# Performance work log

Hardware: AMD Instinct MI355X
Metric: run time of the kernel (lower is better)

## Reference

```python
import jax, jax.numpy as jnp
from jax import lax
import numpy as np

V, H, D, B, W = 256, 512, 2, 256, 256  # vector_size, hidden_size, depth, batch, window_size


def setup_inputs() -> dict:
    key = jax.random.key(0)
    ks = jax.random.split(key, 13)
    scale = 0.04  # ~ 1/sqrt(hidden)
    names = ["w_ih_ltr", "w_hh_ltr", "b_ih_ltr", "b_hh_ltr", "w_fc_ltr", "b_fc_ltr",
             "w_ih_rtl", "w_hh_rtl", "b_ih_rtl", "b_hh_rtl", "w_fc_rtl", "b_fc_rtl"]
    shapes = [(D, 4 * H, V), (D, 4 * H, H), (D, 4 * H), (D, 4 * H), (D, V, H), (D, V)] * 2
    inp = {"x": jax.random.normal(ks[0], (B, W, V), dtype=jnp.float32)}
    for i, (n, s) in enumerate(zip(names, shapes)):
        inp[n] = jax.random.normal(ks[i + 1], s, dtype=jnp.float32) * scale
    return inp


def _lstm_cell(x, h, c, wih, whh, bih, bhh):
    # PyTorch gate order: i, f, g, o
    g = x @ wih.T + bih + h @ whh.T + bhh
    i, f, gg, o = jnp.split(g, 4, axis=-1)
    c = jax.nn.sigmoid(f) * c + jax.nn.sigmoid(i) * jnp.tanh(gg)
    h = jax.nn.sigmoid(o) * jnp.tanh(c)
    return h, c


def _run_dir(xs, wih, whh, bih, bhh, wfc, bfc):
    # xs: (T, B, V); depth LSTM(1-step)+FC blocks with persistent (h,c) per depth
    depth = wih.shape[0]
    h0 = jnp.zeros((depth, xs.shape[1], whh.shape[-1]), xs.dtype)

    def step(carry, x):
        h, c = carry
        v = x
        hs, cs = [], []
        for j in range(depth):  # small fixed depth loop
            hj, cj = _lstm_cell(v, h[j], c[j], wih[j], whh[j], bih[j], bhh[j])
            v = hj @ wfc[j].T + bfc[j]
            hs.append(hj)
            cs.append(cj)
        return (jnp.stack(hs), jnp.stack(cs)), v

    _, ys = lax.scan(step, (h0, h0), xs)
    return ys  # (T, B, V)


def reference(x, w_ih_ltr, w_hh_ltr, b_ih_ltr, b_hh_ltr, w_fc_ltr, b_fc_ltr,
              w_ih_rtl, w_hh_rtl, b_ih_rtl, b_hh_rtl, w_fc_rtl, b_fc_rtl):
    Wlen = x.shape[1]
    xs_f = jnp.swapaxes(x[:, :Wlen - 1, :], 0, 1)        # steps i = 0 .. W-2
    xs_b = jnp.swapaxes(x[:, Wlen - 1:0:-1, :], 0, 1)    # steps -(i+1) = W-1 .. 1
    ys_f = _run_dir(xs_f, w_ih_ltr, w_hh_ltr, b_ih_ltr, b_hh_ltr, w_fc_ltr, b_fc_ltr)
    ys_b = _run_dir(xs_b, w_ih_rtl, w_hh_rtl, b_ih_rtl, b_hh_rtl, w_fc_rtl, b_fc_rtl)
    # torch.stack(output, dim=1): forward outputs then backward outputs -> (B, 2*(W-1), V)
    return jnp.swapaxes(jnp.concatenate([ys_f, ys_b], axis=0), 0, 1)
```

## Files before the change

### kernel.cpp

```cpp
#include <hip/hip_runtime.h>
#include <hip/hip_bf16.h>

using bf16   = __bf16;
using bf16x8 = __attribute__((ext_vector_type(8))) __bf16;
using f32x4  = __attribute__((ext_vector_type(4))) float;
using u32x4  = __attribute__((ext_vector_type(4))) unsigned int;

#define TSTEPS 255
#define UNITE  512
#define HPAR   (16*16*512)
#define WA_UNITS_DIR (128*24)
#define WB_UNITS_DIR (128*32)
#define WC_UNITS_DIR (16*16)

#define MFMA(acc, a, b) acc = __builtin_amdgcn_mfma_f32_16x16x32_bf16((a), (b), (acc), 0, 0, 0)

__device__ __forceinline__ float sigmoidf_(float x) { return 1.f / (1.f + __expf(-x)); }
__device__ __forceinline__ float tanhf_(float x) {
    float e = __expf(-2.f * fabsf(x));
    float t = (1.f - e) / (1.f + e);
    return copysignf(t, x);
}

__device__ __forceinline__ void load8_coh(const bf16* ph, const bf16* pl,
                                          u32x4* h, u32x4* l) {
    asm volatile(
        "global_load_dwordx4 %0, %8, off sc0 sc1\n\t"
        "global_load_dwordx4 %1, %8, off offset:1024 sc0 sc1\n\t"
        "global_load_dwordx4 %2, %8, off offset:2048 sc0 sc1\n\t"
        "global_load_dwordx4 %3, %8, off offset:3072 sc0 sc1\n\t"
        "global_load_dwordx4 %4, %9, off sc0 sc1\n\t"
        "global_load_dwordx4 %5, %9, off offset:1024 sc0 sc1\n\t"
        "global_load_dwordx4 %6, %9, off offset:2048 sc0 sc1\n\t"
        "global_load_dwordx4 %7, %9, off offset:3072 sc0 sc1\n\t"
        "s_waitcnt vmcnt(0)"
        : "=&v"(h[0]), "=&v"(h[1]), "=&v"(h[2]), "=&v"(h[3]),
          "=&v"(l[0]), "=&v"(l[1]), "=&v"(l[2]), "=&v"(l[3])
        : "v"(ph), "v"(pl)
        : "memory");
}

__device__ __forceinline__ void storeh_coh(bf16* ph, bf16* pl,
                                           unsigned short vh, unsigned short vl) {
    asm volatile(
        "global_store_short %0, %2, off sc0 sc1\n\t"
        "global_store_short %1, %3, off sc0 sc1"
        :: "v"(ph), "v"(pl), "v"(vh), "v"(vl)
        : "memory");
}

__device__ __forceinline__ void split_store8(const float* __restrict__ src,
                                             bf16* __restrict__ dh, bf16* __restrict__ dl) {
    float f[8];
    *(float4*)f       = *(const float4*)src;
    *(float4*)(f + 4) = *(const float4*)(src + 4);
    bf16x8 oh, ol;
    #pragma unroll
    for (int j = 0; j < 8; ++j) { bf16 h = (bf16)f[j]; oh[j] = h; ol[j] = (bf16)(f[j] - (float)h); }
    *(bf16x8*)dh = oh; *(bf16x8*)dl = ol;
}

__device__ __forceinline__ void gbarrier(unsigned* __restrict__ flags, int bid, unsigned epoch) {
    asm volatile("s_waitcnt vmcnt(0)" ::: "memory");
    __syncthreads();
    if (threadIdx.x == 0)
        asm volatile("global_store_dword %0, %1, off sc0 sc1"
                     :: "v"(&flags[bid]), "v"(epoch) : "memory");
    if (threadIdx.x < 64) {
        const int l = threadIdx.x;
        for (;;) {
            unsigned f0 = __hip_atomic_load(&flags[l],       __ATOMIC_RELAXED, __HIP_MEMORY_SCOPE_AGENT);
            unsigned f1 = __hip_atomic_load(&flags[l + 64],  __ATOMIC_RELAXED, __HIP_MEMORY_SCOPE_AGENT);
            unsigned f2 = __hip_atomic_load(&flags[l + 128], __ATOMIC_RELAXED, __HIP_MEMORY_SCOPE_AGENT);
            unsigned f3 = __hip_atomic_load(&flags[l + 192], __ATOMIC_RELAXED, __HIP_MEMORY_SCOPE_AGENT);
            if (__all(f0 >= epoch && f1 >= epoch && f2 >= epoch && f3 >= epoch)) break;
            __builtin_amdgcn_s_sleep(1);
        }
    }
    __syncthreads();
}


__global__ void k_pack_wa(const float* __restrict__ wihL, const float* __restrict__ whhL,
                          const float* __restrict__ wihR, const float* __restrict__ whhR,
                          bf16* __restrict__ wah, bf16* __restrict__ wal) {
    int gid = blockIdx.x * 256 + threadIdx.x;
    int lane = gid & 63, u = gid >> 6;
    int kb = u % 24; int tn = (u / 24) & 127; int dir = u / 3072;
    int r = lane & 15, q = lane >> 4;
    int n = tn * 16 + r, k = kb * 32 + q * 8;
    const float* wih = dir ? wihR : wihL;
    const float* whh = dir ? whhR : whhL;
    const float* src = (k < 256) ? (wih + (size_t)n * 256 + k)
                                 : (whh + (size_t)n * 512 + (k - 256));
    split_store8(src, wah + (size_t)u * UNITE + lane * 8, wal + (size_t)u * UNITE + lane * 8);
}

__global__ void k_wcomb(const float* __restrict__ wihL, const float* __restrict__ wfcL,
                        const float* __restrict__ wihR, const float* __restrict__ wfcR,
                        float* __restrict__ wcf) {
    size_t gid = (size_t)blockIdx.x * 256 + threadIdx.x;
    int k = gid & 511; int n = (gid >> 9) & 2047; int dir = (int)(gid >> 20);
    const float* wih1 = (dir ? wihR : wihL) + (size_t)2048 * 256;
    const float* wfc0 = (dir ? wfcR : wfcL);
    float s = 0.f;
    #pragma unroll 8
    for (int v = 0; v < 256; ++v)
        s = fmaf(wih1[(size_t)n * 256 + v], wfc0[(size_t)v * 512 + k], s);
    wcf[gid] = s;
}

__global__ void k_pack_wb(const float* __restrict__ whhL, const float* __restrict__ whhR,
                          const float* __restrict__ wcf,
                          bf16* __restrict__ wbh, bf16* __restrict__ wbl) {
    int gid = blockIdx.x * 256 + threadIdx.x;
    int lane = gid & 63, u = gid >> 6;
    int kb = u & 31, tn = (u >> 5) & 127, dir = u >> 12;
    int r = lane & 15, q = lane >> 4;
    int n = tn * 16 + r, k = kb * 32 + q * 8;
    const float* src;
    if (k < 512) {
        src = wcf + ((size_t)dir * 2048 + n) * 512 + k;
    } else {
        const float* whh1 = (dir ? whhR : whhL) + (size_t)2048 * 512;
        src = whh1 + (size_t)n * 512 + (k - 512);
    }
    split_store8(src, wbh + (size_t)u * UNITE + lane * 8, wbl + (size_t)u * UNITE + lane * 8);
}

__global__ void k_pack_wc(const float* __restrict__ wfcL, const float* __restrict__ wfcR,
                          bf16* __restrict__ wch, bf16* __restrict__ wcl) {
    int gid = blockIdx.x * 256 + threadIdx.x;
    int lane = gid & 63, u = gid >> 6;
    int kb = u & 15, tn = (u >> 4) & 15, dir = u >> 8;
    int r = lane & 15, q = lane >> 4;
    int n = tn * 16 + r, k = kb * 32 + q * 8;
    const float* wfc1 = (dir ? wfcR : wfcL) + (size_t)256 * 512;
    split_store8(wfc1 + (size_t)n * 512 + k,
                 wch + (size_t)u * UNITE + lane * 8, wcl + (size_t)u * UNITE + lane * 8);
}

__global__ void k_bias(const float* __restrict__ bihL, const float* __restrict__ bhhL,
                       const float* __restrict__ bfcL, const float* __restrict__ wihL,
                       const float* __restrict__ bihR, const float* __restrict__ bhhR,
                       const float* __restrict__ bfcR, const float* __restrict__ wihR,
                       float* __restrict__ ba, float* __restrict__ bb, float* __restrict__ bc) {
    int gid = blockIdx.x * 256 + threadIdx.x;
    int n = gid & 2047, dir = gid >> 11;
    const float* bih = dir ? bihR : bihL;
    const float* bhh = dir ? bhhR : bhhL;
    const float* bfc = dir ? bfcR : bfcL;
    const float* wih1 = (dir ? wihR : wihL) + (size_t)2048 * 256;
    ba[dir * 2048 + n] = bih[n] + bhh[n];
    float s = bih[2048 + n] + bhh[2048 + n];
    #pragma unroll 8
    for (int v = 0; v < 256; ++v)
        s = fmaf(bfc[v], wih1[(size_t)n * 256 + v], s);
    bb[dir * 2048 + n] = s;
    if (n < 256) bc[dir * 256 + n] = bfc[256 + n];
}

__global__ __launch_bounds__(256) void bilstm_main(
    const float* __restrict__ x,
    const bf16* __restrict__ wah, const bf16* __restrict__ wal,
    const bf16* __restrict__ wbh, const bf16* __restrict__ wbl,
    const bf16* __restrict__ wch, const bf16* __restrict__ wcl,
    bf16* __restrict__ h0pk, bf16* __restrict__ h1pk,
    const float* __restrict__ ba, const float* __restrict__ bb,
    const float* __restrict__ bc, float* __restrict__ out,
    unsigned* __restrict__ flags)
{
    const int bid  = blockIdx.x;
    const int xcd  = bid & 7;
    const int slot = bid >> 3;
    const int mq   = slot >> 3;
    const int p8   = slot & 7;
    const int pairidx = xcd * 8 + p8;
    const int dir  = pairidx & 1;
    const int nslc = pairidx >> 1;
    const int wv   = threadIdx.x >> 6;
    const int lane = threadIdx.x & 63;
    const int r = lane & 15, q = lane >> 4;
    const int tm = mq * 4 + wv;

    const bf16* WAh = wah + (size_t)dir * WA_UNITS_DIR * UNITE;
    const bf16* WAl = wal + (size_t)dir * WA_UNITS_DIR * UNITE;
    const bf16* WBh = wbh + (size_t)dir * WB_UNITS_DIR * UNITE;
    const bf16* WBl = wbl + (size_t)dir * WB_UNITS_DIR * UNITE;
    const bf16* WCh = wch + (size_t)dir * WC_UNITS_DIR * UNITE;
    const bf16* WCl = wcl + (size_t)dir * WC_UNITS_DIR * UNITE;
    bf16* H0 = h0pk + (size_t)dir * 4 * HPAR;
    bf16* H1 = h1pk + (size_t)dir * 4 * HPAR;
    const float* BA = ba + dir * 2048;
    const float* BB = bb + dir * 2048;
    const float* BC = bc + dir * 256;

    const int col = nslc * 16 + r;
    const int blkK = col >> 5;
    const int kl = col & 31;
    const size_t hw_base = (size_t)(tm * 16 + blkK) * UNITE
                         + (size_t)(kl >> 3) * 128 + (size_t)(4 * q) * 8 + (kl & 7);

    const float bia0 = BA[col], bia1 = BA[512 + col], bia2 = BA[1024 + col], bia3 = BA[1536 + col];
    const float bib0 = BB[col], bib1 = BB[512 + col], bib2 = BB[1024 + col], bib3 = BB[1536 + col];

    const int yid = (nslc * 4 + mq) * 4 + wv;
    const int ytm = yid & 15, ytn = (yid >> 4) & 15, ykh = yid >> 8;
    const float byc = (ykh == 0) ? BC[ytn * 16 + r] : 0.f;

    f32x4 c0 = {0.f, 0.f, 0.f, 0.f}, c1 = {0.f, 0.f, 0.f, 0.f};
    unsigned epoch = 0;

    for (int t = 0; t <= TSTEPS; ++t) {
        const int pw = t & 1, pr = pw ^ 1;
        if (t < TSTEPS) {
            const int pos = dir ? (255 - t) : t;
            f32x4 acc[4] = {{0,0,0,0},{0,0,0,0},{0,0,0,0},{0,0,0,0}};
            const float* xp = x + ((size_t)(tm * 16 + r) * 256 + pos) * 256 + q * 8;
            const bf16* ahh_p = H0 + (size_t)pr * 2 * HPAR + (size_t)(tm * 16) * UNITE + lane * 8;
            const bf16* ahl_p = ahh_p + HPAR;
            #pragma unroll
            for (int kb = 0; kb < 8; ++kb) {
                float xf[8];
                *(float4*)xf       = *(const float4*)(xp + kb * 32);
                *(float4*)(xf + 4) = *(const float4*)(xp + kb * 32 + 4);
                bf16x8 axh, axl;
                #pragma unroll
                for (int j = 0; j < 8; ++j) { bf16 h = (bf16)xf[j]; axh[j] = h; axl[j] = (bf16)(xf[j] - (float)h); }
                #pragma unroll
                for (int g = 0; g < 4; ++g) {
                    const size_t wu = ((size_t)((g * 32 + nslc) * 24) + kb) * UNITE + lane * 8;
                    bf16x8 bh = *(const bf16x8*)(WAh + wu);
                    bf16x8 bl = *(const bf16x8*)(WAl + wu);
                    MFMA(acc[g], axh, bh); MFMA(acc[g], axh, bl); MFMA(acc[g], axl, bh);
                }
            }
            #pragma unroll
            for (int kb0 = 0; kb0 < 16; kb0 += 4) {
                u32x4 th[4], tl[4];
                load8_coh(ahh_p + (size_t)kb0 * UNITE, ahl_p + (size_t)kb0 * UNITE, th, tl);
                #pragma unroll
                for (int j = 0; j < 4; ++j) {
                    bf16x8 hh = __builtin_bit_cast(bf16x8, th[j]);
                    bf16x8 hl = __builtin_bit_cast(bf16x8, tl[j]);
                    const int kb = kb0 + j;
                    #pragma unroll
                    for (int g = 0; g < 4; ++g) {
                        const size_t wu = ((size_t)((g * 32 + nslc) * 24) + 8 + kb) * UNITE + lane * 8;
                        bf16x8 bh = *(const bf16x8*)(WAh + wu);
                        bf16x8 bl = *(const bf16x8*)(WAl + wu);
                        MFMA(acc[g], hh, bh); MFMA(acc[g], hh, bl); MFMA(acc[g], hl, bh);
                    }
                }
            }
            bf16* HwH = H0 + (size_t)pw * 2 * HPAR;
            bf16* HwL = HwH + HPAR;
            #pragma unroll
            for (int i = 0; i < 4; ++i) {
                float gi = sigmoidf_(acc[0][i] + bia0);
                float gf = sigmoidf_(acc[1][i] + bia1);
                float gg = tanhf_   (acc[2][i] + bia2);
                float go = sigmoidf_(acc[3][i] + bia3);
                float cc = gf * c0[i] + gi * gg;
                c0[i] = cc;
                float hv = go * tanhf_(cc);
                bf16 hh = (bf16)hv;
                bf16 hl = (bf16)(hv - (float)hh);
                storeh_coh(HwH + hw_base + (size_t)i * 8, HwL + hw_base + (size_t)i * 8,
                           __builtin_bit_cast(unsigned short, hh),
                           __builtin_bit_cast(unsigned short, hl));
            }
        }
        if (t >= 1) {
            const int py = (t - 1) & 1;
            f32x4 acc = {0, 0, 0, 0};
            const bf16* ayh = H1 + (size_t)py * 2 * HPAR
                            + (size_t)(ytm * 16 + ykh * 8) * UNITE + lane * 8;
            const bf16* ayl = ayh + HPAR;
            #pragma unroll
            for (int kk0 = 0; kk0 < 8; kk0 += 4) {
                u32x4 th[4], tl[4];
                load8_coh(ayh + (size_t)kk0 * UNITE, ayl + (size_t)kk0 * UNITE, th, tl);
                #pragma unroll
                for (int j = 0; j < 4; ++j) {
                    const int kb = ykh * 8 + kk0 + j;
                    const size_t wu = (size_t)(ytn * 16 + kb) * UNITE + lane * 8;
                    bf16x8 bh = *(const bf16x8*)(WCh + wu);
                    bf16x8 bl = *(const bf16x8*)(WCl + wu);
                    bf16x8 ah = __builtin_bit_cast(bf16x8, th[j]);
                    bf16x8 al = __builtin_bit_cast(bf16x8, tl[j]);
                    MFMA(acc, ah, bh); MFMA(acc, ah, bl); MFMA(acc, al, bh);
                }
            }
            const int tout = dir ? (255 + (t - 1)) : (t - 1);
            #pragma unroll
            for (int i = 0; i < 4; ++i) {
                size_t oidx = ((size_t)(ytm * 16 + 4 * q + i) * 510 + tout) * 256 + (ytn * 16 + r);
                atomicAdd(out + oidx, acc[i] + byc);
            }
        }
        ++epoch; gbarrier(flags, bid, epoch);
        if (t < TSTEPS) {
            f32x4 acc[4] = {{0,0,0,0},{0,0,0,0},{0,0,0,0},{0,0,0,0}};
            const bf16* a0h = H0 + (size_t)pw * 2 * HPAR + (size_t)(tm * 16) * UNITE + lane * 8;
            const bf16* a0l = a0h + HPAR;
            const bf16* a1h = H1 + (size_t)pr * 2 * HPAR + (size_t)(tm * 16) * UNITE + lane * 8;
            const bf16* a1l = a1h + HPAR;
            #pragma unroll
            for (int kb0 = 0; kb0 < 16; kb0 += 4) {
                u32x4 th[4], tl[4];
                load8_coh(a0h + (size_t)kb0 * UNITE, a0l + (size_t)kb0 * UNITE, th, tl);
                #pragma unroll
                for (int j = 0; j < 4; ++j) {
                    bf16x8 hh = __builtin_bit_cast(bf16x8, th[j]);
                    bf16x8 hl = __builtin_bit_cast(bf16x8, tl[j]);
                    const int kb = kb0 + j;
                    #pragma unroll
                    for (int g = 0; g < 4; ++g) {
                        const size_t wu = ((size_t)((g * 32 + nslc) * 32) + kb) * UNITE + lane * 8;
                        bf16x8 bh = *(const bf16x8*)(WBh + wu);
                        bf16x8 bl = *(const bf16x8*)(WBl + wu);
                        MFMA(acc[g], hh, bh); MFMA(acc[g], hh, bl); MFMA(acc[g], hl, bh);
                    }
                }
            }
            #pragma unroll
            for (int kb0 = 0; kb0 < 16; kb0 += 4) {
                u32x4 th[4], tl[4];
                load8_coh(a1h + (size_t)kb0 * UNITE, a1l + (size_t)kb0 * UNITE, th, tl);
                #pragma unroll
                for (int j = 0; j < 4; ++j) {
                    bf16x8 hh = __builtin_bit_cast(bf16x8, th[j]);
                    bf16x8 hl = __builtin_bit_cast(bf16x8, tl[j]);
                    const int kb = kb0 + j;
                    #pragma unroll
                    for (int g = 0; g < 4; ++g) {
                        const size_t wu = ((size_t)((g * 32 + nslc) * 32) + 16 + kb) * UNITE + lane * 8;
                        bf16x8 bh = *(const bf16x8*)(WBh + wu);
                        bf16x8 bl = *(const bf16x8*)(WBl + wu);
                        MFMA(acc[g], hh, bh); MFMA(acc[g], hh, bl); MFMA(acc[g], hl, bh);
                    }
                }
            }
            bf16* HwH = H1 + (size_t)pw * 2 * HPAR;
            bf16* HwL = HwH + HPAR;
            #pragma unroll
            for (int i = 0; i < 4; ++i) {
                float gi = sigmoidf_(acc[0][i] + bib0);
                float gf = sigmoidf_(acc[1][i] + bib1);
                float gg = tanhf_   (acc[2][i] + bib2);
                float go = sigmoidf_(acc[3][i] + bib3);
                float cc = gf * c1[i] + gi * gg;
                c1[i] = cc;
                float hv = go * tanhf_(cc);
                bf16 hh = (bf16)hv;
                bf16 hl = (bf16)(hv - (float)hh);
                storeh_coh(HwH + hw_base + (size_t)i * 8, HwL + hw_base + (size_t)i * 8,
                           __builtin_bit_cast(unsigned short, hh),
                           __builtin_bit_cast(unsigned short, hl));
            }
        }
        ++epoch; gbarrier(flags, bid, epoch);
    }
}

extern "C" void kernel_launch(void* const* d_in, const int* in_sizes, int n_in,
                              void* d_out, int out_size, void* d_ws, size_t ws_size,
                              hipStream_t stream) {
    (void)in_sizes; (void)n_in; (void)ws_size;
    const float* x    = (const float*)d_in[0];
    const float* wihL = (const float*)d_in[1];
    const float* whhL = (const float*)d_in[2];
    const float* bihL = (const float*)d_in[3];
    const float* bhhL = (const float*)d_in[4];
    const float* wfcL = (const float*)d_in[5];
    const float* bfcL = (const float*)d_in[6];
    const float* wihR = (const float*)d_in[7];
    const float* whhR = (const float*)d_in[8];
    const float* bihR = (const float*)d_in[9];
    const float* bhhR = (const float*)d_in[10];
    const float* wfcR = (const float*)d_in[11];
    const float* bfcR = (const float*)d_in[12];

    char* ws = (char*)d_ws;
    size_t off = 0;
    auto take = [&](size_t bytes) -> char* {
        off = (off + 255) & ~(size_t)255;
        char* p = ws + off;
        off += bytes;
        return p;
    };
    bf16*     WAH = (bf16*)take((size_t)2 * WA_UNITS_DIR * 1024);
    bf16*     WAL = (bf16*)take((size_t)2 * WA_UNITS_DIR * 1024);
    bf16*     WBH = (bf16*)take((size_t)2 * WB_UNITS_DIR * 1024);
    bf16*     WBL = (bf16*)take((size_t)2 * WB_UNITS_DIR * 1024);
    bf16*     WCH = (bf16*)take((size_t)2 * WC_UNITS_DIR * 1024);
    bf16*     WCL = (bf16*)take((size_t)2 * WC_UNITS_DIR * 1024);
    bf16*     H0  = (bf16*)take((size_t)8 * HPAR * 2);
    bf16*     H1  = (bf16*)take((size_t)8 * HPAR * 2);
    float*    WCF = (float*)take((size_t)2 * 2048 * 512 * 4);
    float*    BA  = (float*)take((size_t)2 * 2048 * 4);
    float*    BB  = (float*)take((size_t)2 * 2048 * 4);
    float*    BC  = (float*)take((size_t)2 * 256 * 4);
    unsigned* FLG = (unsigned*)take((size_t)256 * 4);

    hipMemsetAsync(H0, 0, (size_t)8 * HPAR * 2, stream);
    hipMemsetAsync(H1, 0, (size_t)8 * HPAR * 2, stream);
    hipMemsetAsync(FLG, 0, (size_t)256 * 4, stream);
    hipMemsetAsync(d_out, 0, (size_t)out_size * 4, stream);

    k_pack_wa<<<1536, 256, 0, stream>>>(wihL, whhL, wihR, whhR, WAH, WAL);
    k_wcomb  <<<8192, 256, 0, stream>>>(wihL, wfcL, wihR, wfcR, WCF);
    k_pack_wb<<<2048, 256, 0, stream>>>(whhL, whhR, WCF, WBH, WBL);
    k_pack_wc<<<128,  256, 0, stream>>>(wfcL, wfcR, WCH, WCL);
    k_bias   <<<16,   256, 0, stream>>>(bihL, bhhL, bfcL, wihL, bihR, bhhR, bfcR, wihR, BA, BB, BC);

    bilstm_main<<<256, 256, 0, stream>>>(x, WAH, WAL, WBH, WBL, WCH, WCL,
                                         H0, H1, BA, BB, BC, (float*)d_out, FLG);
}
```

Measured before the change: 32.82 ms.

## Remap blocks to batch-tile ownership and stage hidden states through LDS

```diff
diff --git a/kernel.cpp b/kernel.cpp
--- a/kernel.cpp
+++ b/kernel.cpp
@@ -20,24 +20,6 @@
     float e = __expf(-2.f * fabsf(x));
     float t = (1.f - e) / (1.f + e);
     return copysignf(t, x);
-}
-
-__device__ __forceinline__ void load8_coh(const bf16* ph, const bf16* pl,
-                                          u32x4* h, u32x4* l) {
-    asm volatile(
-        "global_load_dwordx4 %0, %8, off sc0 sc1\n\t"
-        "global_load_dwordx4 %1, %8, off offset:1024 sc0 sc1\n\t"
-        "global_load_dwordx4 %2, %8, off offset:2048 sc0 sc1\n\t"
-        "global_load_dwordx4 %3, %8, off offset:3072 sc0 sc1\n\t"
-        "global_load_dwordx4 %4, %9, off sc0 sc1\n\t"
-        "global_load_dwordx4 %5, %9, off offset:1024 sc0 sc1\n\t"
-        "global_load_dwordx4 %6, %9, off offset:2048 sc0 sc1\n\t"
-        "global_load_dwordx4 %7, %9, off offset:3072 sc0 sc1\n\t"
-        "s_waitcnt vmcnt(0)"
-        : "=&v"(h[0]), "=&v"(h[1]), "=&v"(h[2]), "=&v"(h[3]),
-          "=&v"(l[0]), "=&v"(l[1]), "=&v"(l[2]), "=&v"(l[3])
-        : "v"(ph), "v"(pl)
-        : "memory");
 }
 
 __device__ __forceinline__ void storeh_coh(bf16* ph, bf16* pl,
@@ -47,6 +29,42 @@
         "global_store_short %1, %3, off sc0 sc1"
         :: "v"(ph), "v"(pl), "v"(vh), "v"(vl)
         : "memory");
+}
+
+__device__ __forceinline__ void stage32k(const bf16* gh, const bf16* gl,
+                                         bf16* lds, int tid) {
+    u32x4 a0, a1, a2, a3, b0, b1, b2, b3;
+    const bf16* p0 = gh + tid * 8;
+    const bf16* p1 = p0 + 2048;
+    const bf16* p2 = p0 + 4096;
+    const bf16* p3 = p0 + 6144;
+    const bf16* q0 = gl + tid * 8;
+    const bf16* q1 = q0 + 2048;
+    const bf16* q2 = q0 + 4096;
+    const bf16* q3 = q0 + 6144;
+    asm volatile(
+        "global_load_dwordx4 %0, %8, off sc0 sc1\n\t"
+        "global_load_dwordx4 %1, %9, off sc0 sc1\n\t"
+        "global_load_dwordx4 %2, %10, off sc0 sc1\n\t"
+        "global_load_dwordx4 %3, %11, off sc0 sc1\n\t"
+        "global_load_dwordx4 %4, %12, off sc0 sc1\n\t"
+        "global_load_dwordx4 %5, %13, off sc0 sc1\n\t"
+        "global_load_dwordx4 %6, %14, off sc0 sc1\n\t"
+        "global_load_dwordx4 %7, %15, off sc0 sc1\n\t"
+        "s_waitcnt vmcnt(0)"
+        : "=&v"(a0), "=&v"(a1), "=&v"(a2), "=&v"(a3),
+          "=&v"(b0), "=&v"(b1), "=&v"(b2), "=&v"(b3)
+        : "v"(p0), "v"(p1), "v"(p2), "v"(p3),
+          "v"(q0), "v"(q1), "v"(q2), "v"(q3)
+        : "memory");
+    *(u32x4*)(lds + tid * 8)                 = a0;
+    *(u32x4*)(lds + tid * 8 + 2048)          = a1;
+    *(u32x4*)(lds + tid * 8 + 4096)          = a2;
+    *(u32x4*)(lds + tid * 8 + 6144)          = a3;
+    *(u32x4*)(lds + 8192 + tid * 8)          = b0;
+    *(u32x4*)(lds + 8192 + tid * 8 + 2048)   = b1;
+    *(u32x4*)(lds + 8192 + tid * 8 + 4096)   = b2;
+    *(u32x4*)(lds + 8192 + tid * 8 + 6144)   = b3;
 }
 
 __device__ __forceinline__ void split_store8(const float* __restrict__ src,
@@ -171,17 +189,16 @@
     unsigned* __restrict__ flags)
 {
     const int bid  = blockIdx.x;
-    const int xcd  = bid & 7;
-    const int slot = bid >> 3;
-    const int mq   = slot >> 3;
-    const int p8   = slot & 7;
-    const int pairidx = xcd * 8 + p8;
-    const int dir  = pairidx & 1;
-    const int nslc = pairidx >> 1;
-    const int wv   = threadIdx.x >> 6;
-    const int lane = threadIdx.x & 63;
+    const int nslc = bid & 7;
+    const int bq   = (bid >> 3) & 15;
+    const int dir  = bid >> 7;
+    const int tid  = threadIdx.x;
+    const int wv   = tid >> 6;
+    const int lane = tid & 63;
     const int r = lane & 15, q = lane >> 4;
-    const int tm = mq * 4 + wv;
+
+    __shared__ __align__(16) bf16 h0s[16384];
+    __shared__ __align__(16) bf16 h1s[16384];
 
     const bf16* WAh = wah + (size_t)dir * WA_UNITS_DIR * UNITE;
     const bf16* WAl = wal + (size_t)dir * WA_UNITS_DIR * UNITE;
@@ -195,30 +212,32 @@
     const float* BB = bb + dir * 2048;
     const float* BC = bc + dir * 256;
 
-    const int col = nslc * 16 + r;
-    const int blkK = col >> 5;
-    const int kl = col & 31;
-    const size_t hw_base = (size_t)(tm * 16 + blkK) * UNITE
-                         + (size_t)(kl >> 3) * 128 + (size_t)(4 * q) * 8 + (kl & 7);
-
+    const int nbase = nslc * 4 + wv;
+    const int col   = nslc * 64 + wv * 16 + r;
     const float bia0 = BA[col], bia1 = BA[512 + col], bia2 = BA[1024 + col], bia3 = BA[1536 + col];
     const float bib0 = BB[col], bib1 = BB[512 + col], bib2 = BB[1024 + col], bib3 = BB[1536 + col];
 
-    const int yid = (nslc * 4 + mq) * 4 + wv;
-    const int ytm = yid & 15, ytn = (yid >> 4) & 15, ykh = yid >> 8;
-    const float byc = (ykh == 0) ? BC[ytn * 16 + r] : 0.f;
+    const int hunit  = bq * 16 + nslc * 2 + (wv >> 1);
+    const int hw_off = ((wv & 1) * 2 + (r >> 3)) * 128 + q * 32 + (r & 7);
+
+    const int tn  = nslc * 2 + (wv & 1);
+    const float byc = BC[tn * 16 + r];
 
     f32x4 c0 = {0.f, 0.f, 0.f, 0.f}, c1 = {0.f, 0.f, 0.f, 0.f};
     unsigned epoch = 0;
 
+    #pragma unroll
+    for (int k2 = 0; k2 < 8; ++k2) *(u32x4*)(h0s + tid * 8 + k2 * 2048) = (u32x4){0, 0, 0, 0};
+    __syncthreads();
+
     for (int t = 0; t <= TSTEPS; ++t) {
         const int pw = t & 1, pr = pw ^ 1;
+        stage32k(H1 + (size_t)pr * 2 * HPAR + (size_t)bq * 8192,
+                 H1 + (size_t)pr * 2 * HPAR + HPAR + (size_t)bq * 8192, h1s, tid);
         if (t < TSTEPS) {
             const int pos = dir ? (255 - t) : t;
             f32x4 acc[4] = {{0,0,0,0},{0,0,0,0},{0,0,0,0},{0,0,0,0}};
-            const float* xp = x + ((size_t)(tm * 16 + r) * 256 + pos) * 256 + q * 8;
-            const bf16* ahh_p = H0 + (size_t)pr * 2 * HPAR + (size_t)(tm * 16) * UNITE + lane * 8;
-            const bf16* ahl_p = ahh_p + HPAR;
+            const float* xp = x + ((size_t)(bq * 16 + r) * 256 + pos) * 256 + q * 8;
             #pragma unroll
             for (int kb = 0; kb < 8; ++kb) {
                 float xf[8];
@@ -229,32 +248,26 @@
                 for (int j = 0; j < 8; ++j) { bf16 h = (bf16)xf[j]; axh[j] = h; axl[j] = (bf16)(xf[j] - (float)h); }
                 #pragma unroll
                 for (int g = 0; g < 4; ++g) {
-                    const size_t wu = ((size_t)((g * 32 + nslc) * 24) + kb) * UNITE + lane * 8;
+                    const size_t wu = ((size_t)((g * 32 + nbase) * 24 + kb)) * UNITE + lane * 8;
                     bf16x8 bh = *(const bf16x8*)(WAh + wu);
                     bf16x8 bl = *(const bf16x8*)(WAl + wu);
                     MFMA(acc[g], axh, bh); MFMA(acc[g], axh, bl); MFMA(acc[g], axl, bh);
                 }
             }
             #pragma unroll
-            for (int kb0 = 0; kb0 < 16; kb0 += 4) {
-                u32x4 th[4], tl[4];
-                load8_coh(ahh_p + (size_t)kb0 * UNITE, ahl_p + (size_t)kb0 * UNITE, th, tl);
+            for (int hk = 0; hk < 16; ++hk) {
+                bf16x8 ah = *(const bf16x8*)(h0s + hk * 512 + lane * 8);
+                bf16x8 al = *(const bf16x8*)(h0s + 8192 + hk * 512 + lane * 8);
                 #pragma unroll
-                for (int j = 0; j < 4; ++j) {
-                    bf16x8 hh = __builtin_bit_cast(bf16x8, th[j]);
-                    bf16x8 hl = __builtin_bit_cast(bf16x8, tl[j]);
-                    const int kb = kb0 + j;
-                    #pragma unroll
-                    for (int g = 0; g < 4; ++g) {
-                        const size_t wu = ((size_t)((g * 32 + nslc) * 24) + 8 + kb) * UNITE + lane * 8;
-                        bf16x8 bh = *(const bf16x8*)(WAh + wu);
-                        bf16x8 bl = *(const bf16x8*)(WAl + wu);
-                        MFMA(acc[g], hh, bh); MFMA(acc[g], hh, bl); MFMA(acc[g], hl, bh);
-                    }
+                for (int g = 0; g < 4; ++g) {
+                    const size_t wu = ((size_t)((g * 32 + nbase) * 24 + 8 + hk)) * UNITE + lane * 8;
+                    bf16x8 bh = *(const bf16x8*)(WAh + wu);
+                    bf16x8 bl = *(const bf16x8*)(WAl + wu);
+                    MFMA(acc[g], ah, bh); MFMA(acc[g], ah, bl); MFMA(acc[g], al, bh);
                 }
             }
-            bf16* HwH = H0 + (size_t)pw * 2 * HPAR;
-            bf16* HwL = HwH + HPAR;
+            bf16* WH = H0 + (size_t)pw * 2 * HPAR + (size_t)hunit * 512 + hw_off;
+            bf16* WL = WH + HPAR;
             #pragma unroll
             for (int i = 0; i < 4; ++i) {
                 float gi = sigmoidf_(acc[0][i] + bia0);
@@ -266,84 +279,60 @@
                 float hv = go * tanhf_(cc);
                 bf16 hh = (bf16)hv;
                 bf16 hl = (bf16)(hv - (float)hh);
-                storeh_coh(HwH + hw_base + (size_t)i * 8, HwL + hw_base + (size_t)i * 8,
+                storeh_coh(WH + i * 8, WL + i * 8,
                            __builtin_bit_cast(unsigned short, hh),
                            __builtin_bit_cast(unsigned short, hl));
             }
         }
-        if (t >= 1) {
-            const int py = (t - 1) & 1;
-            f32x4 acc = {0, 0, 0, 0};
-            const bf16* ayh = H1 + (size_t)py * 2 * HPAR
-                            + (size_t)(ytm * 16 + ykh * 8) * UNITE + lane * 8;
-            const bf16* ayl = ayh + HPAR;
-            #pragma unroll
-            for (int kk0 = 0; kk0 < 8; kk0 += 4) {
-                u32x4 th[4], tl[4];
-                load8_coh(ayh + (size_t)kk0 * UNITE, ayl + (size_t)kk0 * UNITE, th, tl);
-                #pragma unroll
-                for (int j = 0; j < 4; ++j) {
-                    const int kb = ykh * 8 + kk0 + j;
-                    const size_t wu = (size_t)(ytn * 16 + kb) * UNITE + lane * 8;
-                    bf16x8 bh = *(const bf16x8*)(WCh + wu);
-                    bf16x8 bl = *(const bf16x8*)(WCl + wu);
-                    bf16x8 ah = __builtin_bit_cast(bf16x8, th[j]);
-                    bf16x8 al = __builtin_bit_cast(bf16x8, tl[j]);
-                    MFMA(acc, ah, bh); MFMA(acc, ah, bl); MFMA(acc, al, bh);
-                }
+        __syncthreads();
+        if (t >= 1 && wv < 2) {
+            f32x4 accy = {0, 0, 0, 0};
+            #pragma unroll
+            for (int kb = 0; kb < 16; ++kb) {
+                bf16x8 ah = *(const bf16x8*)(h1s + kb * 512 + lane * 8);
+                bf16x8 al = *(const bf16x8*)(h1s + 8192 + kb * 512 + lane * 8);
+                const size_t wu = ((size_t)(tn * 16 + kb)) * UNITE + lane * 8;
+                bf16x8 bh = *(const bf16x8*)(WCh + wu);
+                bf16x8 bl = *(const bf16x8*)(WCl + wu);
+                MFMA(accy, ah, bh); MFMA(accy, ah, bl); MFMA(accy, al, bh);
             }
             const int tout = dir ? (255 + (t - 1)) : (t - 1);
             #pragma unroll
-            for (int i = 0; i < 4; ++i) {
-                size_t oidx = ((size_t)(ytm * 16 + 4 * q + i) * 510 + tout) * 256 + (ytn * 16 + r);
-                atomicAdd(out + oidx, acc[i] + byc);
-            }
+            for (int i = 0; i < 4; ++i)
+                out[((size_t)(bq * 16 + 4 * q + i) * 510 + tout) * 256 + tn * 16 + r] = accy[i] + byc;
         }
         ++epoch; gbarrier(flags, bid, epoch);
         if (t < TSTEPS) {
+            stage32k(H0 + (size_t)pw * 2 * HPAR + (size_t)bq * 8192,
+                     H0 + (size_t)pw * 2 * HPAR + HPAR + (size_t)bq * 8192, h0s, tid);
+            __syncthreads();
             f32x4 acc[4] = {{0,0,0,0},{0,0,0,0},{0,0,0,0},{0,0,0,0}};
-            const bf16* a0h = H0 + (size_t)pw * 2 * HPAR + (size_t)(tm * 16) * UNITE + lane * 8;
-            const bf16* a0l = a0h + HPAR;
-            const bf16* a1h = H1 + (size_t)pr * 2 * HPAR + (size_t)(tm * 16) * UNITE + lane * 8;
-            const bf16* a1l = a1h + HPAR;
-            #pragma unroll
-            for (int kb0 = 0; kb0 < 16; kb0 += 4) {
-                u32x4 th[4], tl[4];
-                load8_coh(a0h + (size_t)kb0 * UNITE, a0l + (size_t)kb0 * UNITE, th, tl);
+            #pragma unroll
+            for (int hk = 0; hk < 16; ++hk) {
+                bf16x8 ah = *(const bf16x8*)(h0s + hk * 512 + lane * 8);
+                bf16x8 al = *(const bf16x8*)(h0s + 8192 + hk * 512 + lane * 8);
                 #pragma unroll
-                for (int j = 0; j < 4; ++j) {
-                    bf16x8 hh = __builtin_bit_cast(bf16x8, th[j]);
-                    bf16x8 hl = __builtin_bit_cast(bf16x8, tl[j]);
-                    const int kb = kb0 + j;
-                    #pragma unroll
-                    for (int g = 0; g < 4; ++g) {
-                        const size_t wu = ((size_t)((g * 32 + nslc) * 32) + kb) * UNITE + lane * 8;
-                        bf16x8 bh = *(const bf16x8*)(WBh + wu);
-                        bf16x8 bl = *(const bf16x8*)(WBl + wu);
-                        MFMA(acc[g], hh, bh); MFMA(acc[g], hh, bl); MFMA(acc[g], hl, bh);
-                    }
+                for (int g = 0; g < 4; ++g) {
+                    const size_t wu = ((size_t)((g * 32 + nbase) * 32 + hk)) * UNITE + lane * 8;
+                    bf16x8 bh = *(const bf16x8*)(WBh + wu);
+                    bf16x8 bl = *(const bf16x8*)(WBl + wu);
+                    MFMA(acc[g], ah, bh); MFMA(acc[g], ah, bl); MFMA(acc[g], al, bh);
                 }
             }
             #pragma unroll
-            for (int kb0 = 0; kb0 < 16; kb0 += 4) {
-                u32x4 th[4], tl[4];
-                load8_coh(a1h + (size_t)kb0 * UNITE, a1l + (size_t)kb0 * UNITE, th, tl);
+            for (int hk = 0; hk < 16; ++hk) {
+                bf16x8 ah = *(const bf16x8*)(h1s + hk * 512 + lane * 8);
+                bf16x8 al = *(const bf16x8*)(h1s + 8192 + hk * 512 + lane * 8);
                 #pragma unroll
-                for (int j = 0; j < 4; ++j) {
-                    bf16x8 hh = __builtin_bit_cast(bf16x8, th[j]);
-                    bf16x8 hl = __builtin_bit_cast(bf16x8, tl[j]);
-                    const int kb = kb0 + j;
-                    #pragma unroll
-                    for (int g = 0; g < 4; ++g) {
-                        const size_t wu = ((size_t)((g * 32 + nslc) * 32) + 16 + kb) * UNITE + lane * 8;
-                        bf16x8 bh = *(const bf16x8*)(WBh + wu);
-                        bf16x8 bl = *(const bf16x8*)(WBl + wu);
-                        MFMA(acc[g], hh, bh); MFMA(acc[g], hh, bl); MFMA(acc[g], hl, bh);
-                    }
+                for (int g = 0; g < 4; ++g) {
+                    const size_t wu = ((size_t)((g * 32 + nbase) * 32 + 16 + hk)) * UNITE + lane * 8;
+                    bf16x8 bh = *(const bf16x8*)(WBh + wu);
+                    bf16x8 bl = *(const bf16x8*)(WBl + wu);
+                    MFMA(acc[g], ah, bh); MFMA(acc[g], ah, bl); MFMA(acc[g], al, bh);
                 }
             }
-            bf16* HwH = H1 + (size_t)pw * 2 * HPAR;
-            bf16* HwL = HwH + HPAR;
+            bf16* WH = H1 + (size_t)pw * 2 * HPAR + (size_t)hunit * 512 + hw_off;
+            bf16* WL = WH + HPAR;
             #pragma unroll
             for (int i = 0; i < 4; ++i) {
                 float gi = sigmoidf_(acc[0][i] + bib0);
@@ -355,7 +344,7 @@
                 float hv = go * tanhf_(cc);
                 bf16 hh = (bf16)hv;
                 bf16 hl = (bf16)(hv - (float)hh);
-                storeh_coh(HwH + hw_base + (size_t)i * 8, HwL + hw_base + (size_t)i * 8,
+                storeh_coh(WH + i * 8, WL + i * 8,
                            __builtin_bit_cast(unsigned short, hh),
                            __builtin_bit_cast(unsigned short, hl));
             }
```

After: 32.24 ms. About the same (-1.8%).
